# Kernel optimization log

Hardware: AMD Instinct MI355X
Metric: run time of the kernel (lower is better)

Reference implementation:

```python
import jax, jax.numpy as jnp
import numpy as np

N = [100000, 25000, 6250]        # nodes per scale (coarsening pyramid)
F = 128                          # features_per_scale (all equal)
H = 4                            # num_heads (only enters via the score scale)
SCALE = float((F // H) ** 0.5)
OUT = 5                          # out_channels
E_SAME = [1000000, 400000, 100000]
E_INC = [400000, 100000]


def _cross_attn(src, dst, src_feat, n_dst, qW, qb, kW, kb, vW, vb):
    # GAT-style gather -> per-edge score -> segment softmax over dst -> scatter.
    # In the original model dst_feat is zeros, so Q = 0 @ qW + qb; we keep the
    # matmul so qW appears in the autodiff graph (its grad is zero, faithfully).
    K = src_feat @ kW + kb
    V = src_feat @ vW + vb
    Q = jnp.zeros((n_dst, qW.shape[1]), src_feat.dtype) @ qW + qb
    score = (Q[dst] * K[src]).sum(-1) / SCALE            # [E]
    m = jax.ops.segment_max(score, dst, num_segments=n_dst)
    e = jnp.exp(score - m[dst])
    denom = jax.ops.segment_sum(e, dst, num_segments=n_dst)
    attn = e / denom[dst]                                # segment softmax
    return jax.ops.segment_sum(attn[:, None] * V[src], dst, num_segments=n_dst)


def _gcn(src, dst, x, n, W, b):
    # DGL GraphConv, norm='both': D_out^-1/2 -> scatter-sum -> D_in^-1/2 -> linear.
    ones = jnp.ones(src.shape[0], x.dtype)
    deg_out = jnp.clip(jax.ops.segment_sum(ones, src, num_segments=n), 1.0)
    deg_in = jnp.clip(jax.ops.segment_sum(ones, dst, num_segments=n), 1.0)
    h = x * jax.lax.rsqrt(deg_out)[:, None]
    agg = jax.ops.segment_sum(h[src], dst, num_segments=n)
    return (agg * jax.lax.rsqrt(deg_in)[:, None]) @ W + b


def setup_inputs() -> dict:
    key = jax.random.key(0)
    cnt = [0]
    def rkey():
        cnt[0] += 1
        return jax.random.fold_in(key, cnt[0])
    def rn(shape, s=0.05):
        return jax.random.normal(rkey(), shape, jnp.float32) * s
    def ri(n, hi):
        return jax.random.randint(rkey(), (n,), 0, hi, jnp.int32)
    return {
        "X": rn((N[0], F), 1.0),
        "emb_W": rn((F, F)), "emb_b": rn((F,)),
        "gcn_W": rn((3, F, F)), "gcn_b": rn((3, F)),
        "enc_qW": rn((2, F, F)), "enc_qb": rn((2, F)),
        "enc_kW": rn((2, F, F)), "enc_kb": rn((2, F)),
        "enc_vW": rn((2, F, F)), "enc_vb": rn((2, F)),
        "dec_qW": rn((2, F, F)), "dec_qb": rn((2, F)),
        "dec_kW": rn((2, F, F)), "dec_kb": rn((2, F)),
        "dec_vW": rn((2, F, F)), "dec_vb": rn((2, F)),
        "head_W": rn((3, 2 * F, OUT)), "head_b": rn((3, OUT)),
        "g0_src": ri(E_SAME[0], N[0]), "g0_dst": ri(E_SAME[0], N[0]),
        "g1_src": ri(E_SAME[1], N[1]), "g1_dst": ri(E_SAME[1], N[1]),
        "g2_src": ri(E_SAME[2], N[2]), "g2_dst": ri(E_SAME[2], N[2]),
        "inc0_src": ri(E_INC[0], N[0]), "inc0_dst": ri(E_INC[0], N[1]),
        "inc1_src": ri(E_INC[1], N[1]), "inc1_dst": ri(E_INC[1], N[2]),
        "dec0_src": ri(E_INC[1], N[2]), "dec0_dst": ri(E_INC[1], N[1]),
        "dec1_src": ri(E_INC[0], N[1]), "dec1_dst": ri(E_INC[0], N[0]),
    }


def reference(X, emb_W, emb_b, gcn_W, gcn_b,
              enc_qW, enc_qb, enc_kW, enc_kb, enc_vW, enc_vb,
              dec_qW, dec_qb, dec_kW, dec_kb, dec_vW, dec_vb,
              head_W, head_b,
              g0_src, g0_dst, g1_src, g1_dst, g2_src, g2_dst,
              inc0_src, inc0_dst, inc1_src, inc1_dst,
              dec0_src, dec0_dst, dec1_src, dec1_dst):
    h0 = X @ emb_W + emb_b                               # embedding, scale 0
    # encoder: scale 0 -> 1 -> 2
    e1 = _cross_attn(inc0_src, inc0_dst, h0, N[1],
                     enc_qW[0], enc_qb[0], enc_kW[0], enc_kb[0], enc_vW[0], enc_vb[0])
    e2 = _cross_attn(inc1_src, inc1_dst, e1, N[2],
                     enc_qW[1], enc_qb[1], enc_kW[1], enc_kb[1], enc_vW[1], enc_vb[1])
    feats = [h0, e1, e2]
    edges = [(g0_src, g0_dst), (g1_src, g1_dst), (g2_src, g2_dst)]
    gcn_out = [_gcn(s, d, feats[i], N[i], gcn_W[i], gcn_b[i])
               for i, (s, d) in enumerate(edges)]
    # decoder: scale 2 -> 1 -> 0
    d1 = _cross_attn(dec0_src, dec0_dst, gcn_out[2], N[1],
                     dec_qW[0], dec_qb[0], dec_kW[0], dec_kb[0], dec_vW[0], dec_vb[0])
    d0 = _cross_attn(dec1_src, dec1_dst, d1, N[0],
                     dec_qW[1], dec_qb[1], dec_kW[1], dec_kb[1], dec_vW[1], dec_vb[1])
    decoded = [d0, d1, gcn_out[2]]
    outs = [jax.nn.softmax(jnp.concatenate([gcn_out[i], decoded[i]], -1) @ head_W[i] + head_b[i], -1)
            for i in range(3)]
    return jnp.concatenate(outs, 0)                      # [N0+N1+N2, OUT]
```

## Files before the change

### kernel.cpp

```cpp
#include <hip/hip_runtime.h>
#include <math.h>
#include <stdint.h>

#define N0 100000
#define N1 25000
#define N2 6250
#define FD 128

typedef unsigned short u16;
typedef unsigned int u32;
typedef short bf16x8 __attribute__((ext_vector_type(8)));
typedef float f32x4 __attribute__((ext_vector_type(4)));

static inline int ceildiv(int a, int b){ return (a + b - 1)/b; }

__device__ __forceinline__ u16 f2bf(float f){
  u32 u = __float_as_uint(f);
  u += 0x7fffu + ((u >> 16) & 1u);
  return (u16)(u >> 16);
}
__device__ __forceinline__ float bf2f(u16 h){
  return __uint_as_float(((u32)h) << 16);
}
__device__ __forceinline__ float blo(u32 u){ return __uint_as_float(u << 16); }
__device__ __forceinline__ float bhi(u32 u){ return __uint_as_float(u & 0xffff0000u); }
__device__ __forceinline__ u32 pk2(float a, float b){ return (u32)f2bf(a) | ((u32)f2bf(b) << 16); }

struct BMeta {
  const int* key[10];
  const int* src[7];
  int* rowp[7]; int* csr[7];
  float* rsout[3];
  int n[10], E[10], B[10], r[10];
  int eoff[8];
  int soff[4];
  int boff[11];
  int pblk[11];
};

__device__ __forceinline__ void mm_inner(const float* Al, const float* Wl, int r0, int c0, float acc[4][4]){
  #pragma unroll
  for (int kq = 0; kq < 8; ++kq) {
    int k0 = kq*4;
    float4 a[4], w[4];
    #pragma unroll
    for (int i=0;i<4;++i) a[i] = *(const float4*)&Al[(r0+i)*32 + k0];
    #pragma unroll
    for (int kk=0;kk<4;++kk) w[kk] = *(const float4*)&Wl[(k0+kk)*128 + c0];
    #pragma unroll
    for (int i=0;i<4;++i){
      acc[i][0] = fmaf(a[i].x,w[0].x, fmaf(a[i].y,w[1].x, fmaf(a[i].z,w[2].x, fmaf(a[i].w,w[3].x, acc[i][0]))));
      acc[i][1] = fmaf(a[i].x,w[0].y, fmaf(a[i].y,w[1].y, fmaf(a[i].z,w[2].y, fmaf(a[i].w,w[3].y, acc[i][1]))));
      acc[i][2] = fmaf(a[i].x,w[0].z, fmaf(a[i].y,w[1].z, fmaf(a[i].z,w[2].z, fmaf(a[i].w,w[3].z, acc[i][2]))));
      acc[i][3] = fmaf(a[i].x,w[0].w, fmaf(a[i].y,w[1].w, fmaf(a[i].z,w[2].w, fmaf(a[i].w,w[3].w, acc[i][3]))));
    }
  }
}

template<int SCORE, int AB16>
__device__ __forceinline__ void dev_gemm(float* Wl, float* Al, int bid,
    const void* __restrict__ Ap,
    const float* __restrict__ W, const float* __restrict__ bias,
    const float* __restrict__ kvec, float* __restrict__ sOut,
    u16* __restrict__ out, int n)
{
  const int tid = threadIdx.x;
  const int row0 = bid * 32;
  const int c0 = (tid & 31) * 4, r0 = (tid >> 5) * 4;
  const int r = tid >> 3, fc = tid & 7;
  const int gr_s = row0 + r;
  float acc[4][4] = {};
  float sacc = 0.f;
  const float4* W4 = (const float4*)W;
  for (int kp = 0; kp < 4; ++kp) {
    float4* Wl4 = (float4*)Wl;
    #pragma unroll
    for (int i = 0; i < 4; ++i) Wl4[tid + 256*i] = W4[kp*1024 + tid + 256*i];
    {
      float4 v = make_float4(0.f,0.f,0.f,0.f);
      if (gr_s < n){
        if (AB16){
          ushort4 h = ((const ushort4*)Ap)[(size_t)gr_s*32 + kp*8 + fc];
          v = make_float4(bf2f(h.x), bf2f(h.y), bf2f(h.z), bf2f(h.w));
        } else {
          v = ((const float4*)Ap)[(size_t)gr_s*32 + kp*8 + fc];
        }
      }
      ((float4*)Al)[tid] = v;
      if (SCORE){
        float4 kv = *(const float4*)&kvec[kp*32 + fc*4];
        sacc += v.x*kv.x + v.y*kv.y + v.z*kv.z + v.w*kv.w;
      }
    }
    __syncthreads();
    mm_inner(Al, Wl, r0, c0, acc);
    __syncthreads();
  }
  if (SCORE){
    sacc += __shfl_xor(sacc, 1);
    sacc += __shfl_xor(sacc, 2);
    sacc += __shfl_xor(sacc, 4);
    if (fc == 0 && gr_s < n) sOut[gr_s] = expf(sacc + kvec[128]);
  }
  float4 bv = make_float4(0.f,0.f,0.f,0.f);
  if (bias) bv = *(const float4*)&bias[c0];
  #pragma unroll
  for (int i=0;i<4;++i){
    int gr = row0 + r0 + i;
    if (gr < n){
      ushort4 o;
      o.x = f2bf(acc[i][0]+bv.x); o.y = f2bf(acc[i][1]+bv.y);
      o.z = f2bf(acc[i][2]+bv.z); o.w = f2bf(acc[i][3]+bv.w);
      *(ushort4*)&out[(size_t)gr*FD + c0] = o;
    }
  }
}


__device__ __forceinline__ void dev_dual_mfma(int bid,
    const u16* __restrict__ A, const u16* __restrict__ WvT, const u16* __restrict__ WgT,
    const float* __restrict__ vb, const float* __restrict__ kvec, float* __restrict__ sOut,
    u16* __restrict__ Vout, u16* __restrict__ Yout, int n)
{
  const int tid = threadIdx.x;
  const int wid = tid >> 6, lane = tid & 63;
  const int l15 = lane & 15, lg = lane >> 4;
  const int rt = wid & 1;
  const int cbase = (wid >> 1) * 64;
  const int row0 = bid * 32;
  const int arow = row0 + rt*16 + l15;
  const int arowc = min(arow, n-1);
  f32x4 accV[4] = {{0.f,0.f,0.f,0.f},{0.f,0.f,0.f,0.f},{0.f,0.f,0.f,0.f},{0.f,0.f,0.f,0.f}};
  f32x4 accY[4] = {{0.f,0.f,0.f,0.f},{0.f,0.f,0.f,0.f},{0.f,0.f,0.f,0.f},{0.f,0.f,0.f,0.f}};
  float sacc = 0.f;
  #pragma unroll
  for (int ks = 0; ks < 4; ++ks){
    const int ko = ks*32 + lg*8;
    bf16x8 a = *(const bf16x8*)(A + (size_t)arowc*FD + ko);
    if (wid < 2){
      float4 k0 = *(const float4*)(kvec + ko);
      float4 k1 = *(const float4*)(kvec + ko + 4);
      sacc += bf2f((u16)a[0])*k0.x + bf2f((u16)a[1])*k0.y + bf2f((u16)a[2])*k0.z + bf2f((u16)a[3])*k0.w
            + bf2f((u16)a[4])*k1.x + bf2f((u16)a[5])*k1.y + bf2f((u16)a[6])*k1.z + bf2f((u16)a[7])*k1.w;
    }
    #pragma unroll
    for (int ct = 0; ct < 4; ++ct){
      const int col = cbase + ct*16 + l15;
      bf16x8 bv = *(const bf16x8*)(WvT + (size_t)col*FD + ko);
      bf16x8 bg = *(const bf16x8*)(WgT + (size_t)col*FD + ko);
      accV[ct] = __builtin_amdgcn_mfma_f32_16x16x32_bf16(a, bv, accV[ct], 0, 0, 0);
      accY[ct] = __builtin_amdgcn_mfma_f32_16x16x32_bf16(a, bg, accY[ct], 0, 0, 0);
    }
  }
  if (wid < 2){
    sacc += __shfl_xor(sacc, 16);
    sacc += __shfl_xor(sacc, 32);
    if (lane < 16 && arow < n) sOut[arow] = expf(sacc + kvec[128]);
  }
  #pragma unroll
  for (int ct = 0; ct < 4; ++ct){
    const int col = cbase + ct*16 + l15;
    const float bvv = vb[col];
    #pragma unroll
    for (int i = 0; i < 4; ++i){
      int gr = row0 + rt*16 + lg*4 + i;
      if (gr < n){
        Vout[(size_t)gr*FD + col] = f2bf(accV[ct][i] + bvv);
        Yout[(size_t)gr*FD + col] = f2bf(accY[ct][i]);
      }
    }
  }
}

template<int AF32, int SCORE>
__device__ __forceinline__ void dev_single_mfma(int bid,
    const void* __restrict__ Ap, const u16* __restrict__ WT,
    const float* __restrict__ bias,
    const float* __restrict__ kvec, float* __restrict__ sOut,
    u16* __restrict__ out, int n)
{
  const int tid = threadIdx.x;
  const int wid = tid >> 6, lane = tid & 63;
  const int l15 = lane & 15, lg = lane >> 4;
  const int rt = wid & 1;
  const int cbase = (wid >> 1) * 64;
  const int row0 = bid * 32;
  const int arow = row0 + rt*16 + l15;
  const int arowc = min(arow, n-1);
  f32x4 acc[4] = {{0.f,0.f,0.f,0.f},{0.f,0.f,0.f,0.f},{0.f,0.f,0.f,0.f},{0.f,0.f,0.f,0.f}};
  float sacc = 0.f;
  #pragma unroll
  for (int ks = 0; ks < 4; ++ks){
    const int ko = ks*32 + lg*8;
    bf16x8 a;
    if (AF32){
      const float* Af = (const float*)Ap + (size_t)arowc*FD + ko;
      float4 f0 = *(const float4*)Af;
      float4 f1 = *(const float4*)(Af + 4);
      a[0]=(short)f2bf(f0.x); a[1]=(short)f2bf(f0.y); a[2]=(short)f2bf(f0.z); a[3]=(short)f2bf(f0.w);
      a[4]=(short)f2bf(f1.x); a[5]=(short)f2bf(f1.y); a[6]=(short)f2bf(f1.z); a[7]=(short)f2bf(f1.w);
      if (SCORE && wid < 2){
        float4 k0 = *(const float4*)(kvec + ko);
        float4 k1 = *(const float4*)(kvec + ko + 4);
        sacc += f0.x*k0.x + f0.y*k0.y + f0.z*k0.z + f0.w*k0.w
              + f1.x*k1.x + f1.y*k1.y + f1.z*k1.z + f1.w*k1.w;
      }
    } else {
      a = *(const bf16x8*)((const u16*)Ap + (size_t)arowc*FD + ko);
      if (SCORE && wid < 2){
        float4 k0 = *(const float4*)(kvec + ko);
        float4 k1 = *(const float4*)(kvec + ko + 4);
        sacc += bf2f((u16)a[0])*k0.x + bf2f((u16)a[1])*k0.y + bf2f((u16)a[2])*k0.z + bf2f((u16)a[3])*k0.w
              + bf2f((u16)a[4])*k1.x + bf2f((u16)a[5])*k1.y + bf2f((u16)a[6])*k1.z + bf2f((u16)a[7])*k1.w;
      }
    }
    #pragma unroll
    for (int ct = 0; ct < 4; ++ct){
      const int col = cbase + ct*16 + l15;
      bf16x8 bv = *(const bf16x8*)(WT + (size_t)col*FD + ko);
      acc[ct] = __builtin_amdgcn_mfma_f32_16x16x32_bf16(a, bv, acc[ct], 0, 0, 0);
    }
  }
  if (SCORE && wid < 2){
    sacc += __shfl_xor(sacc, 16);
    sacc += __shfl_xor(sacc, 32);
    if (lane < 16 && arow < n) sOut[arow] = expf(sacc + kvec[128]);
  }
  #pragma unroll
  for (int ct = 0; ct < 4; ++ct){
    const int col = cbase + ct*16 + l15;
    const float bvv = bias[col];
    #pragma unroll
    for (int i = 0; i < 4; ++i){
      int gr = row0 + rt*16 + lg*4 + i;
      if (gr < n) out[(size_t)gr*FD + col] = f2bf(acc[ct][i] + bvv);
    }
  }
}

__device__ __forceinline__ int job_of_blk(const BMeta& m, int bid){
  int j = 0;
  #pragma unroll
  for (int t = 1; t < 10; ++t) if (bid >= m.pblk[t]) j = t;
  return j;
}

__device__ __forceinline__ void dev_p0(const BMeta& m, int bid, int* __restrict__ bktCnt, int* sh){
  int j = job_of_blk(m, bid);
  int lb = bid - m.pblk[j];
  const int* key = m.key[j]; int E = m.E[j], r = m.r[j], B = m.B[j];
  if (threadIdx.x < 64) sh[threadIdx.x] = 0;
  __syncthreads();
  int base = lb*4096 + threadIdx.x;
  #pragma unroll
  for (int i = 0; i < 16; ++i){ int e = base + i*256; if (e < E) atomicAdd(&sh[key[e]/r], 1); }
  __syncthreads();
  if ((int)threadIdx.x < B) atomicAdd(&bktCnt[m.boff[j] + threadIdx.x], sh[threadIdx.x]);
}

__device__ __forceinline__ void dev_p1(const BMeta& m, const int* __restrict__ bktCnt,
    int* __restrict__ bktBase, int* __restrict__ bktCur, int* sh){
  int tid = threadIdx.x;
  for (int i = tid; i < 328; i += 256) sh[i] = bktCnt[i];
  __syncthreads();
  if (tid < 10){
    int acc = (tid < 7) ? m.eoff[tid] : m.soff[tid-7];
    for (int b = m.boff[tid]; b < m.boff[tid+1]; ++b){ int v = sh[b]; sh[b] = acc; acc += v; }
  }
  __syncthreads();
  for (int i = tid; i < 328; i += 256){ bktBase[i] = sh[i]; bktCur[i] = sh[i]; }
}

__device__ __forceinline__ void dev_p2(const BMeta& m, int bid, int* __restrict__ bktCur,
    u32* __restrict__ ebuf, u16* __restrict__ ebuf16, int* sh){
  int j = job_of_blk(m, bid);
  int lb = bid - m.pblk[j];
  const int* key = m.key[j];
  int E = m.E[j], r = m.r[j], B = m.B[j];
  int* h = sh; int* start = sh + 64;
  if (threadIdx.x < 64) h[threadIdx.x] = 0;
  __syncthreads();
  int base = lb*4096 + threadIdx.x;
  #pragma unroll
  for (int i = 0; i < 16; ++i){ int e = base + i*256; if (e < E) atomicAdd(&h[key[e]/r], 1); }
  __syncthreads();
  if ((int)threadIdx.x < B) start[threadIdx.x] = atomicAdd(&bktCur[m.boff[j] + threadIdx.x], h[threadIdx.x]);
  __syncthreads();
  if (j < 7){
    const int* src = m.src[j];
    #pragma unroll
    for (int i = 0; i < 16; ++i){
      int e = base + i*256;
      if (e < E){
        int s = src[e], d = key[e];
        int b = d / r;
        int pos = atomicAdd(&start[b], 1);
        ebuf[pos] = ((u32)(d - b*r) << 17) | (u32)s;
      }
    }
  } else {
    #pragma unroll
    for (int i = 0; i < 16; ++i){
      int e = base + i*256;
      if (e < E){
        int k = key[e];
        int b = k / r;
        int pos = atomicAdd(&start[b], 1);
        ebuf16[pos] = (u16)(k - b*r);
      }
    }
  }
}

__device__ __forceinline__ void dev_p3(const BMeta& m, int bb,
    const int* __restrict__ bktCnt, const int* __restrict__ bktBase,
    const u32* __restrict__ ebuf, const u16* __restrict__ ebuf16, int* sh){
  int j = 0;
  #pragma unroll
  for (int t = 1; t < 10; ++t) if (bb >= m.boff[t]) j = t;
  int b = bb - m.boff[j];
  int n = m.n[j], r = m.r[j];
  int node0 = b*r;
  int rr = min(r, n - node0);
  int gbase = bktBase[bb];
  int cnt = bktCnt[bb];
  int tid = threadIdx.x;
  if (j >= 7){
    int* hist = sh;
    for (int i = tid; i < rr; i += 256) hist[i] = 0;
    __syncthreads();
    for (int e = tid; e < cnt; e += 256) atomicAdd(&hist[ebuf16[gbase + e]], 1);
    __syncthreads();
    float* rs = m.rsout[j-7];
    for (int i = tid; i < rr; i += 256) rs[node0 + i] = rsqrtf(fmaxf((float)hist[i], 1.f));
    return;
  }
  int B = m.B[j];
  int* rowp = m.rowp[j]; int* csr = m.csr[j];
  int lbase = gbase - m.eoff[j];
  int* hist = sh; int* aux = sh + 1568;
  for (int i = tid; i < rr; i += 256) hist[i] = 0;
  __syncthreads();
  for (int e = tid; e < cnt; e += 256){ u32 pk = ebuf[gbase + e]; atomicAdd(&hist[pk >> 17], 1); }
  __syncthreads();
  int ch = (rr + 255) >> 8;
  int i0 = tid*ch;
  int s = 0;
  for (int k = 0; k < ch; ++k){ int idx = i0 + k; if (idx < rr){ int t = hist[idx]; hist[idx] = s; s += t; } }
  aux[tid] = s; __syncthreads();
  for (int off = 1; off < 256; off <<= 1){
    int v = aux[tid]; int a = (tid >= off) ? aux[tid - off] : 0;
    __syncthreads();
    aux[tid] = v + a;
    __syncthreads();
  }
  int pre = (tid ? aux[tid-1] : 0) + lbase;
  for (int k = 0; k < ch; ++k){ int idx = i0 + k; if (idx < rr) hist[idx] += pre; }
  __syncthreads();
  for (int i = tid; i < rr; i += 256) rowp[node0 + i] = hist[i];
  if (b == B-1 && tid == 0) rowp[n] = lbase + cnt;
  __syncthreads();
  for (int e = tid; e < cnt; e += 256){
    u32 pk = ebuf[gbase + e];
    int pos = atomicAdd(&hist[pk >> 17], 1);
    csr[pos] = (int)(pk & 0x1FFFFu);
  }
}

template<int OB16>
__device__ __forceinline__ void dev_attn_gather16(int bid,
    const int* __restrict__ csr, const int* __restrict__ rowp,
    const float* __restrict__ w, const u16* __restrict__ V,
    void* __restrict__ out, int n)
{
  int g = threadIdx.x >> 4, lane = threadIdx.x & 15;
  int row = bid*16 + g;
  if (row >= n) return;
  int st = rowp[row], en = rowp[row+1];
  float a0=0,a1=0,a2=0,a3=0,a4=0,a5=0,a6=0,a7=0;
  if (en > st){
    const uint4* V8 = (const uint4*)V;
    float den = 0.f;
    for (int e = st; e < en; ++e){
      int sn = csr[e];
      float x = w[sn];
      uint4 v = V8[(size_t)sn*16 + lane];
      den += x;
      a0 = fmaf(x, blo(v.x), a0); a1 = fmaf(x, bhi(v.x), a1);
      a2 = fmaf(x, blo(v.y), a2); a3 = fmaf(x, bhi(v.y), a3);
      a4 = fmaf(x, blo(v.z), a4); a5 = fmaf(x, bhi(v.z), a5);
      a6 = fmaf(x, blo(v.w), a6); a7 = fmaf(x, bhi(v.w), a7);
    }
    float inv = 1.f/den;
    a0*=inv; a1*=inv; a2*=inv; a3*=inv; a4*=inv; a5*=inv; a6*=inv; a7*=inv;
  }
  if (OB16){
    uint4 o; o.x = pk2(a0,a1); o.y = pk2(a2,a3); o.z = pk2(a4,a5); o.w = pk2(a6,a7);
    ((uint4*)out)[(size_t)row*16 + lane] = o;
  } else {
    float4* o4 = (float4*)out;
    o4[(size_t)row*32 + lane*2]     = make_float4(a0,a1,a2,a3);
    o4[(size_t)row*32 + lane*2 + 1] = make_float4(a4,a5,a6,a7);
  }
}

template<int OB16>
__device__ __forceinline__ void dev_gcn_gather16(int bid,
    const int* __restrict__ csr, const int* __restrict__ rowp,
    const float* __restrict__ rs, const u16* __restrict__ Y,
    const float* __restrict__ bias, void* __restrict__ out, int n)
{
  int g = threadIdx.x >> 4, lane = threadIdx.x & 15;
  int row = bid*16 + g;
  if (row >= n) return;
  int st = rowp[row], en = rowp[row+1];
  float a0=0,a1=0,a2=0,a3=0,a4=0,a5=0,a6=0,a7=0;
  const uint4* Y8 = (const uint4*)Y;
  for (int e = st; e < en; ++e){
    int sn = csr[e];
    float x = rs[sn];
    uint4 v = Y8[(size_t)sn*16 + lane];
    a0 = fmaf(x, blo(v.x), a0); a1 = fmaf(x, bhi(v.x), a1);
    a2 = fmaf(x, blo(v.y), a2); a3 = fmaf(x, bhi(v.y), a3);
    a4 = fmaf(x, blo(v.z), a4); a5 = fmaf(x, bhi(v.z), a5);
    a6 = fmaf(x, blo(v.w), a6); a7 = fmaf(x, bhi(v.w), a7);
  }
  float sc = rsqrtf(fmaxf((float)(en - st), 1.f));
  const float4* b4 = (const float4*)bias;
  float4 ba = b4[lane*2], bb = b4[lane*2+1];
  float o0=fmaf(a0,sc,ba.x), o1=fmaf(a1,sc,ba.y), o2=fmaf(a2,sc,ba.z), o3=fmaf(a3,sc,ba.w);
  float o4v=fmaf(a4,sc,bb.x), o5=fmaf(a5,sc,bb.y), o6=fmaf(a6,sc,bb.z), o7=fmaf(a7,sc,bb.w);
  if (OB16){
    uint4 o; o.x = pk2(o0,o1); o.y = pk2(o2,o3); o.z = pk2(o4v,o5); o.w = pk2(o6,o7);
    ((uint4*)out)[(size_t)row*16 + lane] = o;
  } else {
    float4* o4 = (float4*)out;
    o4[(size_t)row*32 + lane*2]     = make_float4(o0,o1,o2,o3);
    o4[(size_t)row*32 + lane*2 + 1] = make_float4(o4v,o5,o6,o7);
  }
}

template<int GB16, int DB16>
__device__ __forceinline__ void dev_head(int bid, const void* __restrict__ g, const void* __restrict__ dch,
    const float* __restrict__ W, const float* __restrict__ b,
    float* __restrict__ out, int n, int rowOff)
{
  int wid = threadIdx.x >> 6, lane = threadIdx.x & 63;
  int row = bid*4 + wid;
  if (row >= n) return;
  float x0, x1, x2, x3;
  if (GB16){ const u16* gr = (const u16*)g + (size_t)row*FD; x0 = bf2f(gr[lane]); x1 = bf2f(gr[64+lane]); }
  else     { const float* gr = (const float*)g + (size_t)row*FD; x0 = gr[lane]; x1 = gr[64+lane]; }
  if (DB16){ const u16* dr = (const u16*)dch + (size_t)row*FD; x2 = bf2f(dr[lane]); x3 = bf2f(dr[64+lane]); }
  else     { const float* dr = (const float*)dch + (size_t)row*FD; x2 = dr[lane]; x3 = dr[64+lane]; }
  float acc[5];
  #pragma unroll
  for (int o = 0; o < 5; ++o)
    acc[o] = x0*W[lane*5+o] + x1*W[(64+lane)*5+o] + x2*W[(128+lane)*5+o] + x3*W[(192+lane)*5+o];
  #pragma unroll
  for (int o = 0; o < 5; ++o)
    #pragma unroll
    for (int s = 32; s; s >>= 1) acc[o] += __shfl_xor(acc[o], s);
  if (lane == 0){
    float m = -1e30f;
    #pragma unroll
    for (int o = 0; o < 5; ++o){ acc[o] += b[o]; m = fmaxf(m, acc[o]); }
    float sum = 0.f;
    #pragma unroll
    for (int o = 0; o < 5; ++o){ acc[o] = expf(acc[o]-m); sum += acc[o]; }
    float is = 1.0f/sum;
    float* op = out + (size_t)(rowOff+row)*5;
    #pragma unroll
    for (int o = 0; o < 5; ++o) op[o] = acc[o]*is;
  }
}


__global__ __launch_bounds__(256) void k1_prep(int* __restrict__ zeroBlk, int ntot,
    const float* __restrict__ ekW, const float* __restrict__ ekb, const float* __restrict__ eqb,
    const float* __restrict__ dkW, const float* __restrict__ dkb, const float* __restrict__ dqb,
    float* __restrict__ kv, float inv,
    const float* __restrict__ evW, const float* __restrict__ gW,
    const float* __restrict__ embW, const float* __restrict__ dvW,
    u16* __restrict__ wvt0, u16* __restrict__ wgt0, u16* __restrict__ wvt1, u16* __restrict__ wgt1,
    u16* __restrict__ wembT, u16* __restrict__ wvtd1)
{
  int bid = blockIdx.x;
  if (bid < 4){
    if (threadIdx.x < 128){
      int j = bid;
      const float* kW = (j < 2) ? ekW + j*16384 : dkW + (j-2)*16384;
      const float* kb = (j < 2) ? ekb + j*128   : dkb + (j-2)*128;
      const float* qb = (j < 2) ? eqb + j*128   : dqb + (j-2)*128;
      float* o = kv + j*132;
      int k = threadIdx.x;
      float a = 0.f;
      for (int t = 0; t < 128; ++t) a = fmaf(kW[k*128+t], qb[t], a);
      o[k] = a * inv;
      if (k == 0){
        float c = 0.f;
        for (int t = 0; t < 128; ++t) c = fmaf(kb[t], qb[t], c);
        o[128] = c * inv;
      }
    }
  } else if (bid < 10){
    const float* Ws; u16* Wd;
    if (bid == 4){ Ws = evW;            Wd = wvt0; }
    else if (bid == 5){ Ws = gW;        Wd = wgt0; }
    else if (bid == 6){ Ws = evW+16384; Wd = wvt1; }
    else if (bid == 7){ Ws = gW+16384;  Wd = wgt1; }
    else if (bid == 8){ Ws = embW;      Wd = wembT; }
    else              { Ws = dvW+16384; Wd = wvtd1; }
    for (int i = threadIdx.x; i < 16384; i += 256){
      int k = i >> 7, c = i & 127;
      Wd[c*128 + k] = f2bf(Ws[i]);
    }
  } else {
    int i = (bid-10)*256 + threadIdx.x;
    if (i < ntot) zeroBlk[i] = 0;
  }
}

__global__ __launch_bounds__(256) void k2_p0_gemm(BMeta m, int* __restrict__ bktCnt,
    const float* __restrict__ X, const u16* __restrict__ wembT, const float* __restrict__ b,
    u16* __restrict__ bh0, int np0)
{
  __shared__ int sh[64];
  int bid = blockIdx.x;
  if (bid < np0) dev_p0(m, bid, bktCnt, sh);
  else dev_single_mfma<1,0>(bid - np0, X, wembT, b, nullptr, nullptr, bh0, N0);
}

__global__ __launch_bounds__(256) void k3_p1(BMeta m,
    const int* __restrict__ bktCnt, int* __restrict__ bktBase, int* __restrict__ bktCur)
{
  __shared__ int sh[384];
  dev_p1(m, bktCnt, bktBase, bktCur, sh);
}

__global__ __launch_bounds__(256) void k4_p2_dual(BMeta m, int* __restrict__ bktCur,
    u32* __restrict__ ebuf, u16* __restrict__ ebuf16,
    const u16* __restrict__ bh0,
    const u16* __restrict__ wvt0, const u16* __restrict__ wgt0, const float* __restrict__ evb,
    const float* __restrict__ kvec, float* __restrict__ sS, u16* __restrict__ bV, u16* __restrict__ bY0,
    int np2, int gOff)
{
  __shared__ int sh[1824];
  int bid = blockIdx.x;
  if (bid < np2) dev_p2(m, bid, bktCur, ebuf, ebuf16, sh);
  else dev_dual_mfma(gOff + bid - np2, bh0, wvt0, wgt0, evb, kvec, sS, bV, bY0, N0);
}

__global__ __launch_bounds__(256) void k5_p3_dual(BMeta m,
    const int* __restrict__ bktCnt, const int* __restrict__ bktBase,
    const u32* __restrict__ ebuf, const u16* __restrict__ ebuf16,
    const u16* __restrict__ bh0,
    const u16* __restrict__ wvt0, const u16* __restrict__ wgt0, const float* __restrict__ evb,
    const float* __restrict__ kvec, float* __restrict__ sS, u16* __restrict__ bV, u16* __restrict__ bY0,
    int np3, int gOff)
{
  __shared__ int sh[1824];
  int bid = blockIdx.x;
  if (bid < np3) dev_p3(m, bid, bktCnt, bktBase, ebuf, ebuf16, sh);
  else dev_dual_mfma(gOff + bid - np3, bh0, wvt0, wgt0, evb, kvec, sS, bV, bY0, N0);
}

__global__ __launch_bounds__(256) void k6_ag_i0(
    const int* __restrict__ csrA, const int* __restrict__ rowpA,
    const float* __restrict__ sS, const u16* __restrict__ bV, u16* __restrict__ be1,
    const int* __restrict__ csr0, const int* __restrict__ rowp0, const float* __restrict__ rs0,
    const u16* __restrict__ bY0, const float* __restrict__ gb, u16* __restrict__ bg0, int nMain, int sBase)
{
  int bid = blockIdx.x;
  if (bid < nMain) dev_attn_gather16<1>(bid, csrA, rowpA, sS, bV, be1, N1);
  else dev_gcn_gather16<1>(sBase + bid - nMain, csr0, rowp0, rs0, bY0, gb, bg0, N0);
}

__global__ __launch_bounds__(256) void k7_dual_enc1(
    const u16* __restrict__ be1,
    const u16* __restrict__ wvt1, const u16* __restrict__ wgt1, const float* __restrict__ vb,
    const float* __restrict__ kvec, float* __restrict__ sS, u16* __restrict__ bV, u16* __restrict__ bY1,
    const int* __restrict__ csr0, const int* __restrict__ rowp0, const float* __restrict__ rs0,
    const u16* __restrict__ bY0, const float* __restrict__ gb, u16* __restrict__ bg0, int nMain, int sBase)
{
  int bid = blockIdx.x;
  if (bid < nMain) dev_dual_mfma(bid, be1, wvt1, wgt1, vb, kvec, sS, bV, bY1, N1);
  else dev_gcn_gather16<1>(sBase + bid - nMain, csr0, rowp0, rs0, bY0, gb, bg0, N0);
}

__global__ __launch_bounds__(256) void k8_ag_i1(
    const int* __restrict__ csrA, const int* __restrict__ rowpA,
    const float* __restrict__ sS, const u16* __restrict__ bV, float* __restrict__ be2,
    const int* __restrict__ csr0, const int* __restrict__ rowp0, const float* __restrict__ rs0,
    const u16* __restrict__ bY0, const float* __restrict__ gb, u16* __restrict__ bg0, int nMain, int sBase)
{
  int bid = blockIdx.x;
  if (bid < nMain) dev_attn_gather16<0>(bid, csrA, rowpA, sS, bV, be2, N2);
  else dev_gcn_gather16<1>(sBase + bid - nMain, csr0, rowp0, rs0, bY0, gb, bg0, N0);
}

__global__ __launch_bounds__(256) void k9_y2_g1(
    const float* __restrict__ be2, const float* __restrict__ W2, u16* __restrict__ bY2,
    const int* __restrict__ csr1, const int* __restrict__ rowp1, const float* __restrict__ rs1,
    const u16* __restrict__ bY1, const float* __restrict__ b1, u16* __restrict__ bg1,
    const int* __restrict__ csr0, const int* __restrict__ rowp0, const float* __restrict__ rs0,
    const u16* __restrict__ bY0, const float* __restrict__ gb, u16* __restrict__ bg0,
    int ngemm, int nMain, int sBase)
{
  __shared__ float sm[5120];
  int bid = blockIdx.x;
  if (bid < ngemm) dev_gemm<0,0>(sm, sm+4096, bid, be2, W2, nullptr, nullptr, nullptr, bY2, N2);
  else if (bid < nMain) dev_gcn_gather16<1>(bid - ngemm, csr1, rowp1, rs1, bY1, b1, bg1, N1);
  else dev_gcn_gather16<1>(sBase + bid - nMain, csr0, rowp0, rs0, bY0, gb, bg0, N0);
}

__global__ __launch_bounds__(256) void k10_g2(
    const int* __restrict__ csr2, const int* __restrict__ rowp2, const float* __restrict__ rs2,
    const u16* __restrict__ bY2, const float* __restrict__ b2, float* __restrict__ bg2,
    const int* __restrict__ csr0, const int* __restrict__ rowp0, const float* __restrict__ rs0,
    const u16* __restrict__ bY0, const float* __restrict__ gb, u16* __restrict__ bg0, int nMain, int sBase)
{
  int bid = blockIdx.x;
  if (bid < nMain) dev_gcn_gather16<0>(bid, csr2, rowp2, rs2, bY2, b2, bg2, N2);
  else dev_gcn_gather16<1>(sBase + bid - nMain, csr0, rowp0, rs0, bY0, gb, bg0, N0);
}

__global__ __launch_bounds__(256) void k11_dec0_head2(
    const float* __restrict__ bg2, const float* __restrict__ vW, const float* __restrict__ vb,
    const float* __restrict__ kvec, float* __restrict__ sS, u16* __restrict__ bV,
    const float* __restrict__ hW, const float* __restrict__ hb, float* __restrict__ out,
    const int* __restrict__ csr0, const int* __restrict__ rowp0, const float* __restrict__ rs0,
    const u16* __restrict__ bY0, const float* __restrict__ gb, u16* __restrict__ bg0,
    int ngemm, int nMain, int sBase)
{
  __shared__ float sm[5120];
  int bid = blockIdx.x;
  if (bid < ngemm) dev_gemm<1,0>(sm, sm+4096, bid, bg2, vW, vb, kvec, sS, bV, N2);
  else if (bid < nMain) dev_head<0,0>(bid - ngemm, bg2, bg2, hW, hb, out, N2, N0+N1);
  else dev_gcn_gather16<1>(sBase + bid - nMain, csr0, rowp0, rs0, bY0, gb, bg0, N0);
}

__global__ __launch_bounds__(256) void k12_ag_d1(
    const int* __restrict__ csrA, const int* __restrict__ rowpA,
    const float* __restrict__ sS, const u16* __restrict__ bV, u16* __restrict__ be1,
    const int* __restrict__ csr0, const int* __restrict__ rowp0, const float* __restrict__ rs0,
    const u16* __restrict__ bY0, const float* __restrict__ gb, u16* __restrict__ bg0, int nMain, int sBase)
{
  int bid = blockIdx.x;
  if (bid < nMain) dev_attn_gather16<1>(bid, csrA, rowpA, sS, bV, be1, N1);
  else dev_gcn_gather16<1>(sBase + bid - nMain, csr0, rowp0, rs0, bY0, gb, bg0, N0);
}

__global__ __launch_bounds__(256) void k13_dec1_head1(
    const u16* __restrict__ be1, const u16* __restrict__ wvtd1, const float* __restrict__ vb,
    const float* __restrict__ kvec, float* __restrict__ sS, u16* __restrict__ bV,
    const u16* __restrict__ bg1, const float* __restrict__ hW, const float* __restrict__ hb,
    float* __restrict__ out,
    const int* __restrict__ csr0, const int* __restrict__ rowp0, const float* __restrict__ rs0,
    const u16* __restrict__ bY0, const float* __restrict__ gb, u16* __restrict__ bg0,
    int ngemm, int nMain, int sBase)
{
  int bid = blockIdx.x;
  if (bid < ngemm) dev_single_mfma<0,1>(bid, be1, wvtd1, vb, kvec, sS, bV, N1);
  else if (bid < nMain) dev_head<1,1>(bid - ngemm, bg1, be1, hW, hb, out, N1, N0);
  else dev_gcn_gather16<1>(sBase + bid - nMain, csr0, rowp0, rs0, bY0, gb, bg0, N0);
}

__global__ __launch_bounds__(256) void k14_gather_head0(
    const int* __restrict__ csr, const int* __restrict__ rowp,
    const float* __restrict__ w, const u16* __restrict__ V,
    const u16* __restrict__ bg0,
    const float* __restrict__ hW, const float* __restrict__ hb,
    float* __restrict__ out)
{
  int g = threadIdx.x >> 4, lane = threadIdx.x & 15;
  int row = blockIdx.x*16 + g;
  if (row >= N0) return;
  int st = rowp[row], en = rowp[row+1];
  float a0=0,a1=0,a2=0,a3=0,a4=0,a5=0,a6=0,a7=0;
  if (en > st){
    const uint4* V8 = (const uint4*)V;
    float den = 0.f;
    for (int e = st; e < en; ++e){
      int sn = csr[e];
      float x = w[sn];
      uint4 v = V8[(size_t)sn*16 + lane];
      den += x;
      a0 = fmaf(x, blo(v.x), a0); a1 = fmaf(x, bhi(v.x), a1);
      a2 = fmaf(x, blo(v.y), a2); a3 = fmaf(x, bhi(v.y), a3);
      a4 = fmaf(x, blo(v.z), a4); a5 = fmaf(x, bhi(v.z), a5);
      a6 = fmaf(x, blo(v.w), a6); a7 = fmaf(x, bhi(v.w), a7);
    }
    float inv = 1.f/den;
    a0*=inv; a1*=inv; a2*=inv; a3*=inv; a4*=inv; a5*=inv; a6*=inv; a7*=inv;
  }
  uint4 gv = ((const uint4*)(bg0 + (size_t)row*FD))[lane];
  float g0 = blo(gv.x), g1 = bhi(gv.x), g2 = blo(gv.y), g3 = bhi(gv.y);
  float g4 = blo(gv.z), g5 = bhi(gv.z), g6 = blo(gv.w), g7 = bhi(gv.w);
  int j = 8*lane;
  float acc[5];
  #pragma unroll
  for (int o = 0; o < 5; ++o){
    acc[o] = g0*hW[(j+0)*5+o] + g1*hW[(j+1)*5+o] + g2*hW[(j+2)*5+o] + g3*hW[(j+3)*5+o]
           + g4*hW[(j+4)*5+o] + g5*hW[(j+5)*5+o] + g6*hW[(j+6)*5+o] + g7*hW[(j+7)*5+o]
           + a0*hW[(128+j+0)*5+o] + a1*hW[(128+j+1)*5+o] + a2*hW[(128+j+2)*5+o] + a3*hW[(128+j+3)*5+o]
           + a4*hW[(128+j+4)*5+o] + a5*hW[(128+j+5)*5+o] + a6*hW[(128+j+6)*5+o] + a7*hW[(128+j+7)*5+o];
  }
  #pragma unroll
  for (int o = 0; o < 5; ++o)
    #pragma unroll
    for (int s = 8; s; s >>= 1) acc[o] += __shfl_xor(acc[o], s, 16);
  if (lane == 0){
    float m = -1e30f;
    #pragma unroll
    for (int o = 0; o < 5; ++o){ acc[o] += hb[o]; m = fmaxf(m, acc[o]); }
    float sum = 0.f;
    #pragma unroll
    for (int o = 0; o < 5; ++o){ acc[o] = expf(acc[o]-m); sum += acc[o]; }
    float is = 1.0f/sum;
    float* op = out + (size_t)row*5;
    #pragma unroll
    for (int o = 0; o < 5; ++o) op[o] = acc[o]*is;
  }
}

extern "C" void kernel_launch(void* const* d_in, const int* in_sizes, int n_in,
                              void* d_out, int out_size, void* d_ws, size_t ws_size,
                              hipStream_t stream)
{
  const float* X      = (const float*)d_in[0];
  const float* emb_W  = (const float*)d_in[1];
  const float* emb_b  = (const float*)d_in[2];
  const float* gcn_W  = (const float*)d_in[3];
  const float* gcn_b  = (const float*)d_in[4];
  const float* enc_qb = (const float*)d_in[6];
  const float* enc_kW = (const float*)d_in[7];
  const float* enc_kb = (const float*)d_in[8];
  const float* enc_vW = (const float*)d_in[9];
  const float* enc_vb = (const float*)d_in[10];
  const float* dec_qb = (const float*)d_in[12];
  const float* dec_kW = (const float*)d_in[13];
  const float* dec_kb = (const float*)d_in[14];
  const float* dec_vW = (const float*)d_in[15];
  const float* dec_vb = (const float*)d_in[16];
  const float* head_W = (const float*)d_in[17];
  const float* head_b = (const float*)d_in[18];
  const int* g0s  = (const int*)d_in[19];
  const int* g0d  = (const int*)d_in[20];
  const int* g1s  = (const int*)d_in[21];
  const int* g1d  = (const int*)d_in[22];
  const int* g2s  = (const int*)d_in[23];
  const int* g2d  = (const int*)d_in[24];
  const int* i0s  = (const int*)d_in[25];
  const int* i0d  = (const int*)d_in[26];
  const int* i1s  = (const int*)d_in[27];
  const int* i1d  = (const int*)d_in[28];
  const int* dc0s = (const int*)d_in[29];
  const int* dc0d = (const int*)d_in[30];
  const int* dc1s = (const int*)d_in[31];
  const int* dc1d = (const int*)d_in[32];

  float* ws = (float*)d_ws;
  float* sS  = ws;
  float* kvec = sS + N0;
  float* be2 = kvec + 4*132;
  float* bg2 = be2 + (size_t)N2*FD;
  float* rs0 = bg2 + (size_t)N2*FD;
  float* rs1 = rs0 + N0;
  float* rs2 = rs1 + N1;
  u16*  bh0 = (u16*)(rs2 + N2 + 2);
  u16*  be1 = bh0 + (size_t)N0*FD;
  u16*  bg0 = be1 + (size_t)N1*FD;
  u16*  bg1 = bg0 + (size_t)N0*FD;
  u16*  bV  = bg1 + (size_t)N1*FD;
  u16*  bY0 = bV  + (size_t)N0*FD;
  u16*  bY1 = bV + 4000000;
  u16*  bY2 = bV + 8000000;
  int*  bktCnt  = (int*)(bY0 + (size_t)N0*FD);
  int*  bktBase = bktCnt + 328;
  int*  bktCur  = bktBase + 328;
  int*  rowpBlk = bktCur + 328;
  int*  csrBlk  = rowpBlk + 287507;
  u32*  ebuf    = (u32*)(csrBlk + 2500000);
  u16*  ebuf16  = (u16*)(ebuf + 2500000);
  uintptr_t wtp = ((uintptr_t)(ebuf16 + 1500000) + 15) & ~(uintptr_t)15;
  u16* wvt0 = (u16*)wtp;
  u16* wgt0 = wvt0 + 16384;
  u16* wvt1 = wgt0 + 16384;
  u16* wgt1 = wvt1 + 16384;
  u16* wembT = wgt1 + 16384;
  u16* wvtd1 = wembT + 16384;

  const int* keyP[10] = {g0d,g1d,g2d,i0d,i1d,dc0d,dc1d, g0s,g1s,g2s};
  const int* srcP[7]  = {g0s,g1s,g2s,i0s,i1s,dc0s,dc1s};
  const int nArr[10] = {N0,N1,N2,N1,N2,N1,N0, N0,N1,N2};
  const int EArr[10] = {1000000,400000,100000,400000,100000,100000,400000, 1000000,400000,100000};
  const int BArr[10] = {64,32,8,32,8,16,64, 64,32,8};
  const int rArr[10] = {1563,782,782,782,782,1563,1563, 1563,782,782};

  BMeta m;
  {
    int eo=0, so=0, bo=0, po=0, ro=0, co=0;
    for (int j=0;j<10;++j){
      m.key[j]=keyP[j];
      m.n[j]=nArr[j]; m.E[j]=EArr[j]; m.B[j]=BArr[j]; m.r[j]=rArr[j];
      m.boff[j]=bo; m.pblk[j]=po;
      bo+=BArr[j]; po+=ceildiv(EArr[j],4096);
      if (j < 7){
        m.src[j]=srcP[j]; m.rowp[j]=rowpBlk+ro; m.csr[j]=csrBlk+co;
        m.eoff[j]=eo; eo+=EArr[j]; ro+=nArr[j]+1; co+=EArr[j];
      } else {
        m.soff[j-7]=so; so+=EArr[j];
      }
    }
    m.eoff[7]=eo; m.soff[3]=so; m.boff[10]=bo; m.pblk[10]=po;
  }
  m.rsout[0]=rs0; m.rsout[1]=rs1; m.rsout[2]=rs2;

  const float invScale = 0.17677669529663687f;
  float* out = (float*)d_out;

  const int NP = m.pblk[10];
  const int NB = m.boff[10];
  const int GH0 = ceildiv(N0,32);
  const int GH1 = ceildiv(N1,32);
  const int GH2 = ceildiv(N2,32);
  const int GS1 = 1563;
  const int GA1_16 = ceildiv(N1,16);
  const int GA2_16 = ceildiv(N2,16);
  const int G0B16  = ceildiv(N0,16);
  const int GH2H = ceildiv(N2,4);
  const int GH1H = ceildiv(N1,4);

  int ss[9];
  for (int i = 0; i <= 8; ++i) ss[i] = (int)(((long long)G0B16 * i) / 8);

  k1_prep<<<10 + ceildiv(NB,256), 256, 0, stream>>>(bktCnt, NB,
      enc_kW, enc_kb, enc_qb, dec_kW, dec_kb, dec_qb, kvec, invScale,
      enc_vW, gcn_W, emb_W, dec_vW, wvt0, wgt0, wvt1, wgt1, wembT, wvtd1);
  k2_p0_gemm<<<NP + GH0, 256, 0, stream>>>(m, bktCnt, X, wembT, emb_b, bh0, NP);
  k3_p1<<<1, 256, 0, stream>>>(m, bktCnt, bktBase, bktCur);
  k4_p2_dual<<<NP + GS1, 256, 0, stream>>>(m, bktCur, ebuf, ebuf16,
      bh0, wvt0, wgt0, enc_vb, kvec, sS, bV, bY0, NP, 0);
  k5_p3_dual<<<NB + (GH0 - GS1), 256, 0, stream>>>(m, bktCnt, bktBase, ebuf, ebuf16,
      bh0, wvt0, wgt0, enc_vb, kvec, sS, bV, bY0, NB, GS1);
  k6_ag_i0<<<GA1_16 + (ss[1]-ss[0]), 256, 0, stream>>>(m.csr[3], m.rowp[3], sS, bV, be1,
      m.csr[0], m.rowp[0], rs0, bY0, gcn_b, bg0, GA1_16, ss[0]);
  k7_dual_enc1<<<GH1 + (ss[2]-ss[1]), 256, 0, stream>>>(be1,
      wvt1, wgt1, enc_vb+128, kvec+132, sS, bV, bY1,
      m.csr[0], m.rowp[0], rs0, bY0, gcn_b, bg0, GH1, ss[1]);
  k8_ag_i1<<<GA2_16 + (ss[3]-ss[2]), 256, 0, stream>>>(m.csr[4], m.rowp[4], sS, bV, be2,
      m.csr[0], m.rowp[0], rs0, bY0, gcn_b, bg0, GA2_16, ss[2]);
  k9_y2_g1<<<GH2 + GA1_16 + (ss[4]-ss[3]), 256, 0, stream>>>(be2, gcn_W+32768, bY2,
      m.csr[1], m.rowp[1], rs1, bY1, gcn_b+128, bg1,
      m.csr[0], m.rowp[0], rs0, bY0, gcn_b, bg0, GH2, GH2+GA1_16, ss[3]);
  k10_g2<<<GA2_16 + (ss[5]-ss[4]), 256, 0, stream>>>(m.csr[2], m.rowp[2], rs2, bY2, gcn_b+256, bg2,
      m.csr[0], m.rowp[0], rs0, bY0, gcn_b, bg0, GA2_16, ss[4]);
  k11_dec0_head2<<<GH2 + GH2H + (ss[6]-ss[5]), 256, 0, stream>>>(bg2, dec_vW, dec_vb, kvec+264, sS, bV,
      head_W+2560, head_b+10, out,
      m.csr[0], m.rowp[0], rs0, bY0, gcn_b, bg0, GH2, GH2+GH2H, ss[5]);
  k12_ag_d1<<<GA1_16 + (ss[7]-ss[6]), 256, 0, stream>>>(m.csr[5], m.rowp[5], sS, bV, be1,
      m.csr[0], m.rowp[0], rs0, bY0, gcn_b, bg0, GA1_16, ss[6]);
  k13_dec1_head1<<<GH1 + GH1H + (ss[8]-ss[7]), 256, 0, stream>>>(be1, wvtd1, dec_vb+128, kvec+396, sS, bV,
      bg1, head_W+1280, head_b+5, out,
      m.csr[0], m.rowp[0], rs0, bY0, gcn_b, bg0, GH1, GH1+GH1H, ss[7]);
  k14_gather_head0<<<G0B16, 256, 0, stream>>>(m.csr[6], m.rowp[6], sS, bV, bg0,
      head_W, head_b, out);
}
```

Before: 447.3 us.

## Use per-wave shared histograms in bucketing and unroll gather loops by four

The bucket count and scatter passes now keep a separate shared-memory histogram for each wavefront and compute per-wave start offsets. This cuts LDS atomic contention on the 64 buckets. The gather loops in the attention, GCN and head kernels are unrolled by four, so several independent row loads can be in flight at once. The split of dual-GEMM blocks between the p2 and p3 launches is also retuned, which shifts work between the two kernels.

```diff
diff --git a/kernel.cpp b/kernel.cpp
--- a/kernel.cpp
+++ b/kernel.cpp
@@ -115,7 +115,6 @@
     }
   }
 }
-
 
 __device__ __forceinline__ void dev_dual_mfma(int bid,
     const u16* __restrict__ A, const u16* __restrict__ WvT, const u16* __restrict__ WgT,
@@ -249,13 +248,15 @@
   int j = job_of_blk(m, bid);
   int lb = bid - m.pblk[j];
   const int* key = m.key[j]; int E = m.E[j], r = m.r[j], B = m.B[j];
-  if (threadIdx.x < 64) sh[threadIdx.x] = 0;
-  __syncthreads();
-  int base = lb*4096 + threadIdx.x;
-  #pragma unroll
-  for (int i = 0; i < 16; ++i){ int e = base + i*256; if (e < E) atomicAdd(&sh[key[e]/r], 1); }
-  __syncthreads();
-  if ((int)threadIdx.x < B) atomicAdd(&bktCnt[m.boff[j] + threadIdx.x], sh[threadIdx.x]);
+  int tid = threadIdx.x, wid = tid >> 6;
+  sh[tid] = 0;
+  __syncthreads();
+  int base = lb*4096 + tid;
+  int* wh = sh + wid*64;
+  #pragma unroll
+  for (int i = 0; i < 16; ++i){ int e = base + i*256; if (e < E) atomicAdd(&wh[key[e]/r], 1); }
+  __syncthreads();
+  if (tid < B) atomicAdd(&bktCnt[m.boff[j] + tid], sh[tid] + sh[64+tid] + sh[128+tid] + sh[192+tid]);
 }
 
 __device__ __forceinline__ void dev_p1(const BMeta& m, const int* __restrict__ bktCnt,
@@ -277,15 +278,25 @@
   int lb = bid - m.pblk[j];
   const int* key = m.key[j];
   int E = m.E[j], r = m.r[j], B = m.B[j];
-  int* h = sh; int* start = sh + 64;
-  if (threadIdx.x < 64) h[threadIdx.x] = 0;
-  __syncthreads();
-  int base = lb*4096 + threadIdx.x;
-  #pragma unroll
-  for (int i = 0; i < 16; ++i){ int e = base + i*256; if (e < E) atomicAdd(&h[key[e]/r], 1); }
-  __syncthreads();
-  if ((int)threadIdx.x < B) start[threadIdx.x] = atomicAdd(&bktCur[m.boff[j] + threadIdx.x], h[threadIdx.x]);
-  __syncthreads();
+  int tid = threadIdx.x, wid = tid >> 6;
+  int* wh = sh; int* wstart = sh + 256;
+  wh[tid] = 0;
+  __syncthreads();
+  int base = lb*4096 + tid;
+  int* mywh = wh + wid*64;
+  #pragma unroll
+  for (int i = 0; i < 16; ++i){ int e = base + i*256; if (e < E) atomicAdd(&mywh[key[e]/r], 1); }
+  __syncthreads();
+  if (tid < B){
+    int h0 = wh[tid], h1 = wh[64+tid], h2 = wh[128+tid], h3 = wh[192+tid];
+    int g = atomicAdd(&bktCur[m.boff[j] + tid], h0+h1+h2+h3);
+    wstart[tid] = g;
+    wstart[64+tid] = g + h0;
+    wstart[128+tid] = g + h0 + h1;
+    wstart[192+tid] = g + h0 + h1 + h2;
+  }
+  __syncthreads();
+  int* myst = wstart + wid*64;
   if (j < 7){
     const int* src = m.src[j];
     #pragma unroll
@@ -294,7 +305,7 @@
       if (e < E){
         int s = src[e], d = key[e];
         int b = d / r;
-        int pos = atomicAdd(&start[b], 1);
+        int pos = atomicAdd(&myst[b], 1);
         ebuf[pos] = ((u32)(d - b*r) << 17) | (u32)s;
       }
     }
@@ -305,7 +316,7 @@
       if (e < E){
         int k = key[e];
         int b = k / r;
-        int pos = atomicAdd(&start[b], 1);
+        int pos = atomicAdd(&myst[b], 1);
         ebuf16[pos] = (u16)(k - b*r);
       }
     }
@@ -381,15 +392,29 @@
   if (en > st){
     const uint4* V8 = (const uint4*)V;
     float den = 0.f;
-    for (int e = st; e < en; ++e){
+    int e = st;
+    for (; e + 4 <= en; e += 4){
+      int s0=csr[e], s1=csr[e+1], s2=csr[e+2], s3=csr[e+3];
+      float x0=w[s0], x1=w[s1], x2=w[s2], x3=w[s3];
+      uint4 v0=V8[(size_t)s0*16+lane], v1=V8[(size_t)s1*16+lane];
+      uint4 v2=V8[(size_t)s2*16+lane], v3=V8[(size_t)s3*16+lane];
+      den += x0+x1+x2+x3;
+      a0=fmaf(x0,blo(v0.x),a0); a1=fmaf(x0,bhi(v0.x),a1); a2=fmaf(x0,blo(v0.y),a2); a3=fmaf(x0,bhi(v0.y),a3);
+      a4=fmaf(x0,blo(v0.z),a4); a5=fmaf(x0,bhi(v0.z),a5); a6=fmaf(x0,blo(v0.w),a6); a7=fmaf(x0,bhi(v0.w),a7);
+      a0=fmaf(x1,blo(v1.x),a0); a1=fmaf(x1,bhi(v1.x),a1); a2=fmaf(x1,blo(v1.y),a2); a3=fmaf(x1,bhi(v1.y),a3);
+      a4=fmaf(x1,blo(v1.z),a4); a5=fmaf(x1,bhi(v1.z),a5); a6=fmaf(x1,blo(v1.w),a6); a7=fmaf(x1,bhi(v1.w),a7);
+      a0=fmaf(x2,blo(v2.x),a0); a1=fmaf(x2,bhi(v2.x),a1); a2=fmaf(x2,blo(v2.y),a2); a3=fmaf(x2,bhi(v2.y),a3);
+      a4=fmaf(x2,blo(v2.z),a4); a5=fmaf(x2,bhi(v2.z),a5); a6=fmaf(x2,blo(v2.w),a6); a7=fmaf(x2,bhi(v2.w),a7);
+      a0=fmaf(x3,blo(v3.x),a0); a1=fmaf(x3,bhi(v3.x),a1); a2=fmaf(x3,blo(v3.y),a2); a3=fmaf(x3,bhi(v3.y),a3);
+      a4=fmaf(x3,blo(v3.z),a4); a5=fmaf(x3,bhi(v3.z),a5); a6=fmaf(x3,blo(v3.w),a6); a7=fmaf(x3,bhi(v3.w),a7);
+    }
+    for (; e < en; ++e){
       int sn = csr[e];
       float x = w[sn];
       uint4 v = V8[(size_t)sn*16 + lane];
       den += x;
-      a0 = fmaf(x, blo(v.x), a0); a1 = fmaf(x, bhi(v.x), a1);
-      a2 = fmaf(x, blo(v.y), a2); a3 = fmaf(x, bhi(v.y), a3);
-      a4 = fmaf(x, blo(v.z), a4); a5 = fmaf(x, bhi(v.z), a5);
-      a6 = fmaf(x, blo(v.w), a6); a7 = fmaf(x, bhi(v.w), a7);
+      a0=fmaf(x,blo(v.x),a0); a1=fmaf(x,bhi(v.x),a1); a2=fmaf(x,blo(v.y),a2); a3=fmaf(x,bhi(v.y),a3);
+      a4=fmaf(x,blo(v.z),a4); a5=fmaf(x,bhi(v.z),a5); a6=fmaf(x,blo(v.w),a6); a7=fmaf(x,bhi(v.w),a7);
     }
     float inv = 1.f/den;
     a0*=inv; a1*=inv; a2*=inv; a3*=inv; a4*=inv; a5*=inv; a6*=inv; a7*=inv;
@@ -416,14 +441,27 @@
   int st = rowp[row], en = rowp[row+1];
   float a0=0,a1=0,a2=0,a3=0,a4=0,a5=0,a6=0,a7=0;
   const uint4* Y8 = (const uint4*)Y;
-  for (int e = st; e < en; ++e){
+  int e = st;
+  for (; e + 4 <= en; e += 4){
+    int s0=csr[e], s1=csr[e+1], s2=csr[e+2], s3=csr[e+3];
+    float x0=rs[s0], x1=rs[s1], x2=rs[s2], x3=rs[s3];
+    uint4 v0=Y8[(size_t)s0*16+lane], v1=Y8[(size_t)s1*16+lane];
+    uint4 v2=Y8[(size_t)s2*16+lane], v3=Y8[(size_t)s3*16+lane];
+    a0=fmaf(x0,blo(v0.x),a0); a1=fmaf(x0,bhi(v0.x),a1); a2=fmaf(x0,blo(v0.y),a2); a3=fmaf(x0,bhi(v0.y),a3);
+    a4=fmaf(x0,blo(v0.z),a4); a5=fmaf(x0,bhi(v0.z),a5); a6=fmaf(x0,blo(v0.w),a6); a7=fmaf(x0,bhi(v0.w),a7);
+    a0=fmaf(x1,blo(v1.x),a0); a1=fmaf(x1,bhi(v1.x),a1); a2=fmaf(x1,blo(v1.y),a2); a3=fmaf(x1,bhi(v1.y),a3);
+    a4=fmaf(x1,blo(v1.z),a4); a5=fmaf(x1,bhi(v1.z),a5); a6=fmaf(x1,blo(v1.w),a6); a7=fmaf(x1,bhi(v1.w),a7);
+    a0=fmaf(x2,blo(v2.x),a0); a1=fmaf(x2,bhi(v2.x),a1); a2=fmaf(x2,blo(v2.y),a2); a3=fmaf(x2,bhi(v2.y),a3);
+    a4=fmaf(x2,blo(v2.z),a4); a5=fmaf(x2,bhi(v2.z),a5); a6=fmaf(x2,blo(v2.w),a6); a7=fmaf(x2,bhi(v2.w),a7);
+    a0=fmaf(x3,blo(v3.x),a0); a1=fmaf(x3,bhi(v3.x),a1); a2=fmaf(x3,blo(v3.y),a2); a3=fmaf(x3,bhi(v3.y),a3);
+    a4=fmaf(x3,blo(v3.z),a4); a5=fmaf(x3,bhi(v3.z),a5); a6=fmaf(x3,blo(v3.w),a6); a7=fmaf(x3,bhi(v3.w),a7);
+  }
+  for (; e < en; ++e){
     int sn = csr[e];
     float x = rs[sn];
     uint4 v = Y8[(size_t)sn*16 + lane];
-    a0 = fmaf(x, blo(v.x), a0); a1 = fmaf(x, bhi(v.x), a1);
-    a2 = fmaf(x, blo(v.y), a2); a3 = fmaf(x, bhi(v.y), a3);
-    a4 = fmaf(x, blo(v.z), a4); a5 = fmaf(x, bhi(v.z), a5);
-    a6 = fmaf(x, blo(v.w), a6); a7 = fmaf(x, bhi(v.w), a7);
+    a0=fmaf(x,blo(v.x),a0); a1=fmaf(x,bhi(v.x),a1); a2=fmaf(x,blo(v.y),a2); a3=fmaf(x,bhi(v.y),a3);
+    a4=fmaf(x,blo(v.z),a4); a5=fmaf(x,bhi(v.z),a5); a6=fmaf(x,blo(v.w),a6); a7=fmaf(x,bhi(v.w),a7);
   }
   float sc = rsqrtf(fmaxf((float)(en - st), 1.f));
   const float4* b4 = (const float4*)bias;
@@ -525,7 +563,7 @@
     const float* __restrict__ X, const u16* __restrict__ wembT, const float* __restrict__ b,
     u16* __restrict__ bh0, int np0)
 {
-  __shared__ int sh[64];
+  __shared__ int sh[256];
   int bid = blockIdx.x;
   if (bid < np0) dev_p0(m, bid, bktCnt, sh);
   else dev_single_mfma<1,0>(bid - np0, X, wembT, b, nullptr, nullptr, bh0, N0);
@@ -545,7 +583,7 @@
     const float* __restrict__ kvec, float* __restrict__ sS, u16* __restrict__ bV, u16* __restrict__ bY0,
     int np2, int gOff)
 {
-  __shared__ int sh[1824];
+  __shared__ int sh[512];
   int bid = blockIdx.x;
   if (bid < np2) dev_p2(m, bid, bktCur, ebuf, ebuf16, sh);
   else dev_dual_mfma(gOff + bid - np2, bh0, wvt0, wgt0, evb, kvec, sS, bV, bY0, N0);
@@ -681,15 +719,29 @@
   if (en > st){
     const uint4* V8 = (const uint4*)V;
     float den = 0.f;
-    for (int e = st; e < en; ++e){
+    int e = st;
+    for (; e + 4 <= en; e += 4){
+      int s0=csr[e], s1=csr[e+1], s2=csr[e+2], s3=csr[e+3];
+      float x0=w[s0], x1=w[s1], x2=w[s2], x3=w[s3];
+      uint4 v0=V8[(size_t)s0*16+lane], v1=V8[(size_t)s1*16+lane];
+      uint4 v2=V8[(size_t)s2*16+lane], v3=V8[(size_t)s3*16+lane];
+      den += x0+x1+x2+x3;
+      a0=fmaf(x0,blo(v0.x),a0); a1=fmaf(x0,bhi(v0.x),a1); a2=fmaf(x0,blo(v0.y),a2); a3=fmaf(x0,bhi(v0.y),a3);
+      a4=fmaf(x0,blo(v0.z),a4); a5=fmaf(x0,bhi(v0.z),a5); a6=fmaf(x0,blo(v0.w),a6); a7=fmaf(x0,bhi(v0.w),a7);
+      a0=fmaf(x1,blo(v1.x),a0); a1=fmaf(x1,bhi(v1.x),a1); a2=fmaf(x1,blo(v1.y),a2); a3=fmaf(x1,bhi(v1.y),a3);
+      a4=fmaf(x1,blo(v1.z),a4); a5=fmaf(x1,bhi(v1.z),a5); a6=fmaf(x1,blo(v1.w),a6); a7=fmaf(x1,bhi(v1.w),a7);
+      a0=fmaf(x2,blo(v2.x),a0); a1=fmaf(x2,bhi(v2.x),a1); a2=fmaf(x2,blo(v2.y),a2); a3=fmaf(x2,bhi(v2.y),a3);
+      a4=fmaf(x2,blo(v2.z),a4); a5=fmaf(x2,bhi(v2.z),a5); a6=fmaf(x2,blo(v2.w),a6); a7=fmaf(x2,bhi(v2.w),a7);
+      a0=fmaf(x3,blo(v3.x),a0); a1=fmaf(x3,bhi(v3.x),a1); a2=fmaf(x3,blo(v3.y),a2); a3=fmaf(x3,bhi(v3.y),a3);
+      a4=fmaf(x3,blo(v3.z),a4); a5=fmaf(x3,bhi(v3.z),a5); a6=fmaf(x3,blo(v3.w),a6); a7=fmaf(x3,bhi(v3.w),a7);
+    }
+    for (; e < en; ++e){
       int sn = csr[e];
       float x = w[sn];
       uint4 v = V8[(size_t)sn*16 + lane];
       den += x;
-      a0 = fmaf(x, blo(v.x), a0); a1 = fmaf(x, bhi(v.x), a1);
-      a2 = fmaf(x, blo(v.y), a2); a3 = fmaf(x, bhi(v.y), a3);
-      a4 = fmaf(x, blo(v.z), a4); a5 = fmaf(x, bhi(v.z), a5);
-      a6 = fmaf(x, blo(v.w), a6); a7 = fmaf(x, bhi(v.w), a7);
+      a0=fmaf(x,blo(v.x),a0); a1=fmaf(x,bhi(v.x),a1); a2=fmaf(x,blo(v.y),a2); a3=fmaf(x,bhi(v.y),a3);
+      a4=fmaf(x,blo(v.z),a4); a5=fmaf(x,bhi(v.z),a5); a6=fmaf(x,blo(v.w),a6); a7=fmaf(x,bhi(v.w),a7);
     }
     float inv = 1.f/den;
     a0*=inv; a1*=inv; a2*=inv; a3*=inv; a4*=inv; a5*=inv; a6*=inv; a7*=inv;
@@ -825,7 +877,7 @@
   const int GH0 = ceildiv(N0,32);
   const int GH1 = ceildiv(N1,32);
   const int GH2 = ceildiv(N2,32);
-  const int GS1 = 1563;
+  const int GS1 = 1900;
   const int GA1_16 = ceildiv(N1,16);
   const int GA2_16 = ceildiv(N2,16);
   const int G0B16  = ceildiv(N0,16);
```

After: 417.1 us. -6.8%, faster.
